# Kernel tuning notes

Hardware: AMD Instinct MI355X
Metric: run time of the kernel (lower is better)

Reference implementation:

```python
import jax, jax.numpy as jnp
import numpy as np

B, S, HID = 2, 2048, 4096
NH, NKV, HD = 32, 8, 128
GRP = NH // NKV          # query heads per kv head
G = 128                  # weight quant group size
FP8_MAX = 448.0          # e4m3 max
EPS = 1e-6


def _rmsnorm(x, w):
    return x * jax.lax.rsqrt(jnp.mean(x * x, axis=-1, keepdims=True) + EPS) * w


def _act_quant(x):
    # per-token fp8 quantization: scale = amax/448, values clipped to fp8 range
    s = jnp.max(jnp.abs(x), axis=-1, keepdims=True) / FP8_MAX
    s = jnp.maximum(s, 1e-6)
    return jnp.clip(x / s, -FP8_MAX, FP8_MAX), s


def _deq_weight(wi4, wscale):
    # wi4: [out, in] int values in [0,16) -> signed int4 [-8,7]
    # wscale: [out, in//G] per-group scales, broadcast along input dim
    return (wi4.astype(jnp.float32) - 8.0) * jnp.repeat(wscale, G, axis=1)


def _rotate_half(x):
    x1, x2 = jnp.split(x, 2, axis=-1)
    return jnp.concatenate([-x2, x1], axis=-1)


def setup_inputs() -> dict:
    key = jax.random.key(0)
    ks = jax.random.split(key, 8)
    hidden_states = jax.random.normal(ks[0], (B, S, HID), dtype=jnp.float32)
    ln_weight = jnp.ones((HID,), dtype=jnp.float32)
    # real RoPE tables
    inv_freq = 1.0 / (10000.0 ** (np.arange(0, HD, 2, dtype=np.float32) / HD))
    ang = np.arange(S, dtype=np.float32)[:, None] * inv_freq[None, :]
    emb = np.concatenate([ang, ang], axis=-1)  # [S, HD]
    cos = jnp.broadcast_to(jnp.asarray(np.cos(emb)), (B, S, HD)).astype(jnp.float32)
    sin = jnp.broadcast_to(jnp.asarray(np.sin(emb)), (B, S, HD)).astype(jnp.float32)
    def wq(k, out, inp):
        ki, ksc = jax.random.split(k)
        wi = jax.random.randint(ki, (out, inp), 0, 16, dtype=jnp.int32)
        sc = jax.random.uniform(ksc, (out, inp // G), dtype=jnp.float32) * 0.01 + 0.001
        return wi, sc
    wq_i4, wq_scale = wq(ks[1], NH * HD, HID)
    wk_i4, wk_scale = wq(ks[2], NKV * HD, HID)
    wv_i4, wv_scale = wq(ks[3], NKV * HD, HID)
    wo_i4, wo_scale = wq(ks[4], HID, NH * HD)
    return dict(hidden_states=hidden_states, ln_weight=ln_weight, cos=cos, sin=sin,
                wq_scale=wq_scale, wk_scale=wk_scale, wv_scale=wv_scale, wo_scale=wo_scale,
                wq_i4=wq_i4, wk_i4=wk_i4, wv_i4=wv_i4, wo_i4=wo_i4)


def reference(hidden_states, ln_weight, cos, sin,
              wq_scale, wk_scale, wv_scale, wo_scale,
              wq_i4, wk_i4, wv_i4, wo_i4):
    b, s, _ = hidden_states.shape
    residual = hidden_states
    h = _rmsnorm(hidden_states, ln_weight)
    qx, qx_s = _act_quant(h)                     # [b,s,HID], [b,s,1]
    q = (qx @ _deq_weight(wq_i4, wq_scale).T) * qx_s
    k = (qx @ _deq_weight(wk_i4, wk_scale).T) * qx_s
    v = (qx @ _deq_weight(wv_i4, wv_scale).T) * qx_s
    q = q.reshape(b, s, NH, HD)
    k = k.reshape(b, s, NKV, HD)
    v = v.reshape(b, s, NKV, HD)
    cse, sne = cos[:, :, None, :], sin[:, :, None, :]
    q = q * cse + _rotate_half(q) * sne
    k = k * cse + _rotate_half(k) * sne
    # GQA causal attention (fp8 fmha numerics emulated in fp32)
    qg = q.reshape(b, s, NKV, GRP, HD)
    scaling = HD ** -0.5
    scores = jnp.einsum('bskgd,btkd->bkgst', qg, k) * scaling  # [b,kv,g,s,t]
    causal = jnp.tril(jnp.ones((s, s), dtype=bool))
    scores = jnp.where(causal, scores, jnp.float32(-1e30))
    p = jax.nn.softmax(scores, axis=-1)
    o = jnp.einsum('bkgst,btkd->bskgd', p, v).reshape(b, s, NH * HD)
    qo, qo_s = _act_quant(o)
    out = (qo @ _deq_weight(wo_i4, wo_scale).T) * qo_s + residual
    return out
```

## Files before the change

kernel.cpp:

```cpp
#include <hip/hip_runtime.h>
#include <stdint.h>

#define HID    4096
#define SLEN   2048
#define BATCH  2
#define NHEADS 32
#define NKVH   8
#define HDIM   128
#define NTOK   (BATCH*SLEN)
#define NQK    (NHEADS*HDIM)
#define NKVD   (NKVH*HDIM)
#define NQKV   (NQK + 2*NKVD)
#define ASTR   (NQK + NKVD)

typedef unsigned short u16;
typedef short short8 __attribute__((ext_vector_type(8)));
typedef float f32x4 __attribute__((ext_vector_type(4)));
typedef int int4v __attribute__((ext_vector_type(4)));
typedef u16 u16x4 __attribute__((ext_vector_type(4)));

static __device__ __forceinline__ u16 f2bf(float f) {
  unsigned u = __builtin_bit_cast(unsigned, f);
  u += 0x7FFFu + ((u >> 16) & 1u);
  return (u16)(u >> 16);
}
static __device__ __forceinline__ float bf2f(u16 h) {
  return __builtin_bit_cast(float, (unsigned)h << 16);
}
static __device__ __forceinline__ void gload_lds16(const void* g, void* l) {
  __builtin_amdgcn_global_load_lds((const __attribute__((address_space(1))) void*)g,
                                   (__attribute__((address_space(3))) void*)l, 16, 0, 0);
}

__global__ __launch_bounds__(256) void k_rmsnorm(const float* __restrict__ x,
                                                 const float* __restrict__ w,
                                                 u16* __restrict__ h) {
  const int row = blockIdx.x;
  const float4* xr = (const float4*)(x + (size_t)row * HID);
  float4 vals[4];
  float ss = 0.f;
#pragma unroll
  for (int i = 0; i < 4; ++i) {
    float4 v = xr[threadIdx.x + i * 256];
    vals[i] = v;
    ss += v.x*v.x + v.y*v.y + v.z*v.z + v.w*v.w;
  }
#pragma unroll
  for (int off = 32; off; off >>= 1) ss += __shfl_xor(ss, off);
  __shared__ float red[4];
  if ((threadIdx.x & 63) == 0) red[threadIdx.x >> 6] = ss;
  __syncthreads();
  ss = red[0] + red[1] + red[2] + red[3];
  const float scale = rsqrtf(ss * (1.f / HID) + 1e-6f);
  u16* hr = h + (size_t)row * HID;
#pragma unroll
  for (int i = 0; i < 4; ++i) {
    int c = (threadIdx.x + i * 256) * 4;
    float4 v = vals[i];
    unsigned lo = (unsigned)f2bf(v.x * scale * w[c])   | ((unsigned)f2bf(v.y * scale * w[c+1]) << 16);
    unsigned hi = (unsigned)f2bf(v.z * scale * w[c+2]) | ((unsigned)f2bf(v.w * scale * w[c+3]) << 16);
    *(unsigned long long*)(hr + c) = ((unsigned long long)hi << 32) | lo;
  }
}

__global__ __launch_bounds__(256) void k_deq(const int* __restrict__ W,
                                             const float* __restrict__ Ws,
                                             u16* __restrict__ out) {
  const int idx = blockIdx.x * 256 + threadIdx.x;
  const int n = idx >> 9;
  const int k8 = (idx & 511) * 8;
  const float sc = Ws[n * 32 + (k8 >> 7)];
  int4v a = *(const int4v*)(W + (size_t)n * HID + k8);
  int4v b = *(const int4v*)(W + (size_t)n * HID + k8 + 4);
  u16 r[8];
#pragma unroll
  for (int j = 0; j < 4; ++j) r[j]     = f2bf((float)(a[j] - 8) * sc);
#pragma unroll
  for (int j = 0; j < 4; ++j) r[j + 4] = f2bf((float)(b[j] - 8) * sc);
  *(short8*)(out + (size_t)n * HID + k8) = *(short8*)r;
}

#define BM 128
#define BN 128
#define BK 64

__global__ __launch_bounds__(256) void k_gemm_qkv_b(
    const u16* __restrict__ A, const u16* __restrict__ B,
    u16* __restrict__ C, u16* __restrict__ Vt) {
  __shared__ __align__(16) u16 lA[BM * BK];
  __shared__ __align__(16) u16 lB[BN * BK];
  const int tid = threadIdx.x;
  const int lane = tid & 63;
  const int wave = tid >> 6;
  const int wm = wave >> 1, wn = wave & 1;
  const int m0 = blockIdx.x * BM;
  const int n0 = blockIdx.y * BN;

  const int rloc = wave * 8 + (lane >> 3);
  const int lb8 = (((lane & 7) ^ (lane >> 3)) << 3);

  f32x4 acc[4][4];
#pragma unroll
  for (int mi = 0; mi < 4; ++mi)
#pragma unroll
    for (int ni = 0; ni < 4; ++ni) acc[mi][ni] = (f32x4){0.f, 0.f, 0.f, 0.f};

  for (int k0 = 0; k0 < HID; k0 += BK) {
    __syncthreads();
#pragma unroll
    for (int p = 0; p < 4; ++p)
      gload_lds16(A + (size_t)(m0 + p * 32 + rloc) * HID + k0 + lb8,
                  lA + p * 2048 + wave * 512);
#pragma unroll
    for (int p = 0; p < 4; ++p)
      gload_lds16(B + (size_t)(n0 + p * 32 + rloc) * HID + k0 + lb8,
                  lB + p * 2048 + wave * 512);
    __syncthreads();
#pragma unroll
    for (int kc = 0; kc < 2; ++kc) {
      const int kOff = kc * 32 + ((lane >> 4) << 3);
      short8 af[4], bfr[4];
#pragma unroll
      for (int i = 0; i < 4; ++i) {
        const int m = wm * 64 + i * 16 + (lane & 15);
        af[i] = *(const short8*)(lA + ((m * 64 + kOff) ^ ((m & 7) << 3)));
        const int n = wn * 64 + i * 16 + (lane & 15);
        bfr[i] = *(const short8*)(lB + ((n * 64 + kOff) ^ ((n & 7) << 3)));
      }
#pragma unroll
      for (int mi = 0; mi < 4; ++mi)
#pragma unroll
        for (int ni = 0; ni < 4; ++ni)
          acc[mi][ni] = __builtin_amdgcn_mfma_f32_16x16x32_bf16(af[mi], bfr[ni], acc[mi][ni], 0, 0, 0);
    }
  }
  if (n0 < ASTR) {
#pragma unroll
    for (int mi = 0; mi < 4; ++mi) {
      const int row = m0 + wm * 64 + mi * 16 + ((lane >> 4) << 2);
#pragma unroll
      for (int ni = 0; ni < 4; ++ni) {
        const int col = n0 + wn * 64 + ni * 16 + (lane & 15);
#pragma unroll
        for (int r = 0; r < 4; ++r)
          C[(size_t)(row + r) * ASTR + col] = f2bf(acc[mi][ni][r]);
      }
    }
  } else {
#pragma unroll
    for (int mi = 0; mi < 4; ++mi) {
      const int row = m0 + wm * 64 + mi * 16 + ((lane >> 4) << 2);
      const int b_ = row >> 11, s_ = row & 2047;
#pragma unroll
      for (int ni = 0; ni < 4; ++ni) {
        const int colv = (n0 - ASTR) + wn * 64 + ni * 16 + (lane & 15);
        u16x4 pk;
#pragma unroll
        for (int r = 0; r < 4; ++r) pk[r] = f2bf(acc[mi][ni][r]);
        *(u16x4*)(Vt + ((size_t)(b_ * NKVH + (colv >> 7)) * HDIM + (colv & 127)) * SLEN + s_) = pk;
      }
    }
  }
}

__global__ __launch_bounds__(256) void k_gemm_o_b(
    const u16* __restrict__ A, const u16* __restrict__ B,
    const float* __restrict__ resid, float* __restrict__ out) {
  __shared__ __align__(16) u16 lA[BM * BK];
  __shared__ __align__(16) u16 lB[BN * BK];
  const int tid = threadIdx.x;
  const int lane = tid & 63;
  const int wave = tid >> 6;
  const int wm = wave >> 1, wn = wave & 1;
  const int m0 = blockIdx.x * BM;
  const int n0 = blockIdx.y * BN;

  const int rloc = wave * 8 + (lane >> 3);
  const int lb8 = (((lane & 7) ^ (lane >> 3)) << 3);

  f32x4 acc[4][4];
#pragma unroll
  for (int mi = 0; mi < 4; ++mi)
#pragma unroll
    for (int ni = 0; ni < 4; ++ni) acc[mi][ni] = (f32x4){0.f, 0.f, 0.f, 0.f};

  for (int k0 = 0; k0 < NQK; k0 += BK) {
    __syncthreads();
#pragma unroll
    for (int p = 0; p < 4; ++p)
      gload_lds16(A + (size_t)(m0 + p * 32 + rloc) * NQK + k0 + lb8,
                  lA + p * 2048 + wave * 512);
#pragma unroll
    for (int p = 0; p < 4; ++p)
      gload_lds16(B + (size_t)(n0 + p * 32 + rloc) * NQK + k0 + lb8,
                  lB + p * 2048 + wave * 512);
    __syncthreads();
#pragma unroll
    for (int kc = 0; kc < 2; ++kc) {
      const int kOff = kc * 32 + ((lane >> 4) << 3);
      short8 af[4], bfr[4];
#pragma unroll
      for (int i = 0; i < 4; ++i) {
        const int m = wm * 64 + i * 16 + (lane & 15);
        af[i] = *(const short8*)(lA + ((m * 64 + kOff) ^ ((m & 7) << 3)));
        const int n = wn * 64 + i * 16 + (lane & 15);
        bfr[i] = *(const short8*)(lB + ((n * 64 + kOff) ^ ((n & 7) << 3)));
      }
#pragma unroll
      for (int mi = 0; mi < 4; ++mi)
#pragma unroll
        for (int ni = 0; ni < 4; ++ni)
          acc[mi][ni] = __builtin_amdgcn_mfma_f32_16x16x32_bf16(af[mi], bfr[ni], acc[mi][ni], 0, 0, 0);
    }
  }
#pragma unroll
  for (int mi = 0; mi < 4; ++mi) {
    const int row = m0 + wm * 64 + mi * 16 + ((lane >> 4) << 2);
#pragma unroll
    for (int ni = 0; ni < 4; ++ni) {
      const int col = n0 + wn * 64 + ni * 16 + (lane & 15);
#pragma unroll
      for (int r = 0; r < 4; ++r) {
        const size_t idx = (size_t)(row + r) * HID + col;
        out[idx] = acc[mi][ni][r] + resid[idx];
      }
    }
  }
}

__global__ __launch_bounds__(256) void k_gemm_qkv(
    const u16* __restrict__ A,
    const int* __restrict__ Wq, const int* __restrict__ Wk, const int* __restrict__ Wv,
    const float* __restrict__ Sq, const float* __restrict__ Sk, const float* __restrict__ Sv,
    u16* __restrict__ C, u16* __restrict__ Vt) {
  __shared__ __align__(16) u16 lA[BM * BK];
  __shared__ __align__(16) u16 lB[BN * BK];
  const int tid = threadIdx.x;
  const int lane = tid & 63;
  const int wave = tid >> 6;
  const int wm = wave >> 1, wn = wave & 1;
  const int m0 = blockIdx.x * BM;
  const int n0 = blockIdx.y * BN;

  const int* W; const float* Ws; int nb;
  if (n0 < NQK)       { W = Wq; Ws = Sq; nb = n0; }
  else if (n0 < ASTR) { W = Wk; Ws = Sk; nb = n0 - NQK; }
  else                { W = Wv; Ws = Sv; nb = n0 - ASTR; }

  const int mloc = wave * 8 + (lane >> 3);
  const int lb8 = (((lane & 7) ^ (lane >> 3)) << 3);

  f32x4 acc[4][4];
#pragma unroll
  for (int mi = 0; mi < 4; ++mi)
#pragma unroll
    for (int ni = 0; ni < 4; ++ni) acc[mi][ni] = (f32x4){0.f, 0.f, 0.f, 0.f};

  for (int k0 = 0; k0 < HID; k0 += BK) {
    __syncthreads();
#pragma unroll
    for (int p = 0; p < 4; ++p)
      gload_lds16(A + (size_t)(m0 + p * 32 + mloc) * HID + k0 + lb8,
                  lA + p * 2048 + wave * 512);
    const int grp = k0 >> 7;
#pragma unroll
    for (int p = 0; p < 8; ++p) {
      const int n = p * 16 + (tid >> 4);
      const int kk = (tid & 15) * 4;
      int4v wv4 = *(const int4v*)(W + (size_t)(nb + n) * HID + k0 + kk);
      const float sc = Ws[(nb + n) * 32 + grp];
      unsigned lo = (unsigned)f2bf((float)(wv4[0] - 8) * sc) |
                    ((unsigned)f2bf((float)(wv4[1] - 8) * sc) << 16);
      unsigned hi = (unsigned)f2bf((float)(wv4[2] - 8) * sc) |
                    ((unsigned)f2bf((float)(wv4[3] - 8) * sc) << 16);
      const int di = (n * 64 + kk) ^ ((n & 7) << 3);
      unsigned* dst = (unsigned*)(lB + di);
      dst[0] = lo; dst[1] = hi;
    }
    __syncthreads();
#pragma unroll
    for (int kc = 0; kc < 2; ++kc) {
      const int kOff = kc * 32 + ((lane >> 4) << 3);
      short8 af[4], bfr[4];
#pragma unroll
      for (int i = 0; i < 4; ++i) {
        const int m = wm * 64 + i * 16 + (lane & 15);
        af[i] = *(const short8*)(lA + ((m * 64 + kOff) ^ ((m & 7) << 3)));
        const int n = wn * 64 + i * 16 + (lane & 15);
        bfr[i] = *(const short8*)(lB + ((n * 64 + kOff) ^ ((n & 7) << 3)));
      }
#pragma unroll
      for (int mi = 0; mi < 4; ++mi)
#pragma unroll
        for (int ni = 0; ni < 4; ++ni)
          acc[mi][ni] = __builtin_amdgcn_mfma_f32_16x16x32_bf16(af[mi], bfr[ni], acc[mi][ni], 0, 0, 0);
    }
  }
  if (n0 < ASTR) {
#pragma unroll
    for (int mi = 0; mi < 4; ++mi) {
      const int row = m0 + wm * 64 + mi * 16 + ((lane >> 4) << 2);
#pragma unroll
      for (int ni = 0; ni < 4; ++ni) {
        const int col = n0 + wn * 64 + ni * 16 + (lane & 15);
#pragma unroll
        for (int r = 0; r < 4; ++r)
          C[(size_t)(row + r) * ASTR + col] = f2bf(acc[mi][ni][r]);
      }
    }
  } else {
#pragma unroll
    for (int mi = 0; mi < 4; ++mi) {
      const int row = m0 + wm * 64 + mi * 16 + ((lane >> 4) << 2);
      const int b_ = row >> 11, s_ = row & 2047;
#pragma unroll
      for (int ni = 0; ni < 4; ++ni) {
        const int colv = (n0 - ASTR) + wn * 64 + ni * 16 + (lane & 15);
        u16x4 pk;
#pragma unroll
        for (int r = 0; r < 4; ++r) pk[r] = f2bf(acc[mi][ni][r]);
        *(u16x4*)(Vt + ((size_t)(b_ * NKVH + (colv >> 7)) * HDIM + (colv & 127)) * SLEN + s_) = pk;
      }
    }
  }
}

__global__ __launch_bounds__(256) void k_gemm_o(
    const u16* __restrict__ A, const int* __restrict__ W, const float* __restrict__ Ws,
    const float* __restrict__ resid, float* __restrict__ out) {
  __shared__ __align__(16) u16 lA[BM * BK];
  __shared__ __align__(16) u16 lB[BN * BK];
  const int tid = threadIdx.x;
  const int lane = tid & 63;
  const int wave = tid >> 6;
  const int wm = wave >> 1, wn = wave & 1;
  const int m0 = blockIdx.x * BM;
  const int n0 = blockIdx.y * BN;

  const int mloc = wave * 8 + (lane >> 3);
  const int lb8 = (((lane & 7) ^ (lane >> 3)) << 3);

  f32x4 acc[4][4];
#pragma unroll
  for (int mi = 0; mi < 4; ++mi)
#pragma unroll
    for (int ni = 0; ni < 4; ++ni) acc[mi][ni] = (f32x4){0.f, 0.f, 0.f, 0.f};

  for (int k0 = 0; k0 < NQK; k0 += BK) {
    __syncthreads();
#pragma unroll
    for (int p = 0; p < 4; ++p)
      gload_lds16(A + (size_t)(m0 + p * 32 + mloc) * NQK + k0 + lb8,
                  lA + p * 2048 + wave * 512);
    const int grp = k0 >> 7;
#pragma unroll
    for (int p = 0; p < 8; ++p) {
      const int n = p * 16 + (tid >> 4);
      const int kk = (tid & 15) * 4;
      int4v wv4 = *(const int4v*)(W + (size_t)(n0 + n) * NQK + k0 + kk);
      const float sc = Ws[(n0 + n) * 32 + grp];
      unsigned lo = (unsigned)f2bf((float)(wv4[0] - 8) * sc) |
                    ((unsigned)f2bf((float)(wv4[1] - 8) * sc) << 16);
      unsigned hi = (unsigned)f2bf((float)(wv4[2] - 8) * sc) |
                    ((unsigned)f2bf((float)(wv4[3] - 8) * sc) << 16);
      const int di = (n * 64 + kk) ^ ((n & 7) << 3);
      unsigned* dst = (unsigned*)(lB + di);
      dst[0] = lo; dst[1] = hi;
    }
    __syncthreads();
#pragma unroll
    for (int kc = 0; kc < 2; ++kc) {
      const int kOff = kc * 32 + ((lane >> 4) << 3);
      short8 af[4], bfr[4];
#pragma unroll
      for (int i = 0; i < 4; ++i) {
        const int m = wm * 64 + i * 16 + (lane & 15);
        af[i] = *(const short8*)(lA + ((m * 64 + kOff) ^ ((m & 7) << 3)));
        const int n = wn * 64 + i * 16 + (lane & 15);
        bfr[i] = *(const short8*)(lB + ((n * 64 + kOff) ^ ((n & 7) << 3)));
      }
#pragma unroll
      for (int mi = 0; mi < 4; ++mi)
#pragma unroll
        for (int ni = 0; ni < 4; ++ni)
          acc[mi][ni] = __builtin_amdgcn_mfma_f32_16x16x32_bf16(af[mi], bfr[ni], acc[mi][ni], 0, 0, 0);
      }
  }
#pragma unroll
  for (int mi = 0; mi < 4; ++mi) {
    const int row = m0 + wm * 64 + mi * 16 + ((lane >> 4) << 2);
#pragma unroll
    for (int ni = 0; ni < 4; ++ni) {
      const int col = n0 + wn * 64 + ni * 16 + (lane & 15);
#pragma unroll
      for (int r = 0; r < 4; ++r) {
        const size_t idx = (size_t)(row + r) * HID + col;
        out[idx] = acc[mi][ni][r] + resid[idx];
      }
    }
  }
}

__global__ __launch_bounds__(256) void k_rope(u16* __restrict__ qk,
                                              const float* __restrict__ cosb,
                                              const float* __restrict__ sinb) {
  const int idx = blockIdx.x * 256 + threadIdx.x;
  const int d = idx & 63;
  const int hh = (idx >> 6) % 40;
  const int t = idx / (64 * 40);
  const int col = (hh < 32) ? hh * HDIM : NQK + (hh - 32) * HDIM;
  u16* p = qk + (size_t)t * ASTR + col;
  const float c = cosb[t * HDIM + d], s = sinb[t * HDIM + d];
  const float x1 = bf2f(p[d]), x2 = bf2f(p[d + 64]);
  p[d]      = f2bf(x1 * c - x2 * s);
  p[d + 64] = f2bf(x2 * c + x1 * s);
}

__global__ __launch_bounds__(256) void k_attn(const u16* __restrict__ qk,
                                              const u16* __restrict__ vt,
                                              u16* __restrict__ o) {
  const int slot = blockIdx.x;
  const int w = (slot & 7) * 128 + (slot >> 3);
  const int qi = 15 - (w & 15);
  const int h = (w >> 4) & 31;
  const int b = w >> 9;
  const int kvh = h >> 2;
  const int q0 = qi * 128;
  const int lane = threadIdx.x & 63, wave = threadIdx.x >> 6;
  const int m = lane & 15, kg = lane >> 4;

  const u16* Qb = qk + (size_t)b * SLEN * ASTR + h * HDIM;
  const u16* Kb = qk + (size_t)b * SLEN * ASTR + NQK + kvh * HDIM;
  const u16* Vb = vt + (size_t)(b * NKVH + kvh) * HDIM * SLEN;

  __shared__ __align__(16) u16 Kt[64 * 128];
  __shared__ __align__(16) u16 Vts[128 * 64];
  __shared__ __align__(16) u16 Pl[4][32 * 72];

  const int qr = q0 + wave * 32;
  short8 qf[2][4];
#pragma unroll
  for (int mi = 0; mi < 2; ++mi)
#pragma unroll
    for (int kc = 0; kc < 4; ++kc)
      qf[mi][kc] = *(const short8*)(Qb + (size_t)(qr + mi * 16 + m) * ASTR + kc * 32 + kg * 8);

  f32x4 oacc[2][8];
#pragma unroll
  for (int mi = 0; mi < 2; ++mi)
#pragma unroll
    for (int n = 0; n < 8; ++n) oacc[mi][n] = (f32x4){0.f, 0.f, 0.f, 0.f};
  float rm[2][4], rl[2][4];
#pragma unroll
  for (int mi = 0; mi < 2; ++mi)
#pragma unroll
    for (int r = 0; r < 4; ++r) { rm[mi][r] = -3.0e38f; rl[mi][r] = 0.f; }

  const float sscale = 0.08838834764831845f;
  const int nt = q0 / 64 + 2;
  for (int t = 0; t < nt; ++t) {
    const int kv0 = t * 64;
    __syncthreads();
#pragma unroll
    for (int p = 0; p < 4; ++p) {
      const int row = p * 16 + wave * 4 + (lane >> 4);
      const int c8s = (lane & 15) ^ (row & 7);
      gload_lds16(Kb + (size_t)(kv0 + row) * ASTR + c8s * 8, Kt + p * 2048 + wave * 512);
    }
#pragma unroll
    for (int p = 0; p < 4; ++p) {
      const int d = p * 32 + wave * 8 + (lane >> 3);
      const int c8s = (lane & 7) ^ (d & 7);
      gload_lds16(Vb + (size_t)d * SLEN + kv0 + c8s * 8, Vts + p * 2048 + wave * 512);
    }
    __syncthreads();

    f32x4 sf[2][4];
#pragma unroll
    for (int mi = 0; mi < 2; ++mi)
#pragma unroll
      for (int ni = 0; ni < 4; ++ni) sf[mi][ni] = (f32x4){0.f, 0.f, 0.f, 0.f};
#pragma unroll
    for (int ni = 0; ni < 4; ++ni)
#pragma unroll
      for (int kc = 0; kc < 4; ++kc) {
        const int krow = ni * 16 + m;
        short8 kf = *(const short8*)(Kt + krow * 128 + (((kc * 4 + kg) ^ (krow & 7)) << 3));
#pragma unroll
        for (int mi = 0; mi < 2; ++mi)
          sf[mi][ni] = __builtin_amdgcn_mfma_f32_16x16x32_bf16(qf[mi][kc], kf, sf[mi][ni], 0, 0, 0);
      }

#pragma unroll
    for (int mi = 0; mi < 2; ++mi) {
      const bool dg = (kv0 + 63 > qr + mi * 16);
      float tmax[4] = {-3.0e38f, -3.0e38f, -3.0e38f, -3.0e38f};
#pragma unroll
      for (int ni = 0; ni < 4; ++ni)
#pragma unroll
        for (int r = 0; r < 4; ++r) {
          float s = sf[mi][ni][r] * sscale;
          if (dg) {
            const int rowg = qr + mi * 16 + kg * 4 + r;
            const int colg = kv0 + ni * 16 + m;
            if (colg > rowg) s = -1e30f;
          }
          sf[mi][ni][r] = s;
          tmax[r] = fmaxf(tmax[r], s);
        }
#pragma unroll
      for (int r = 0; r < 4; ++r)
#pragma unroll
        for (int off = 1; off < 16; off <<= 1)
          tmax[r] = fmaxf(tmax[r], __shfl_xor(tmax[r], off));
      float scl[4], psum[4];
#pragma unroll
      for (int r = 0; r < 4; ++r) {
        const float mn = fmaxf(rm[mi][r], tmax[r]);
        scl[r] = __expf(rm[mi][r] - mn);
        rm[mi][r] = mn;
        psum[r] = 0.f;
      }
#pragma unroll
      for (int ni = 0; ni < 4; ++ni)
#pragma unroll
        for (int r = 0; r < 4; ++r) {
          const float p = __expf(sf[mi][ni][r] - rm[mi][r]);
          psum[r] += p;
          Pl[wave][(mi * 16 + kg * 4 + r) * 72 + ni * 16 + m] = f2bf(p);
        }
#pragma unroll
      for (int r = 0; r < 4; ++r) {
#pragma unroll
        for (int off = 1; off < 16; off <<= 1)
          psum[r] += __shfl_xor(psum[r], off);
        rl[mi][r] = rl[mi][r] * scl[r] + psum[r];
      }
#pragma unroll
      for (int n = 0; n < 8; ++n)
#pragma unroll
        for (int r = 0; r < 4; ++r) oacc[mi][n][r] *= scl[r];
    }

#pragma unroll
    for (int kc = 0; kc < 2; ++kc) {
      short8 pf[2];
#pragma unroll
      for (int mi = 0; mi < 2; ++mi)
        pf[mi] = *(const short8*)(&Pl[wave][(mi * 16 + m) * 72 + kc * 32 + kg * 8]);
#pragma unroll
      for (int n = 0; n < 8; ++n) {
        const int vrow = n * 16 + m;
        short8 vf = *(const short8*)(Vts + vrow * 64 + (((kc * 4 + kg) ^ (vrow & 7)) << 3));
#pragma unroll
        for (int mi = 0; mi < 2; ++mi)
          oacc[mi][n] = __builtin_amdgcn_mfma_f32_16x16x32_bf16(pf[mi], vf, oacc[mi][n], 0, 0, 0);
      }
    }
  }

#pragma unroll
  for (int mi = 0; mi < 2; ++mi) {
    float inv[4];
#pragma unroll
    for (int r = 0; r < 4; ++r) inv[r] = 1.0f / rl[mi][r];
#pragma unroll
    for (int n = 0; n < 8; ++n)
#pragma unroll
      for (int r = 0; r < 4; ++r) {
        const int row = qr + mi * 16 + kg * 4 + r;
        o[((size_t)b * SLEN + row) * NQK + h * HDIM + n * 16 + m] = f2bf(oacc[mi][n][r] * inv[r]);
      }
  }
}

extern "C" void kernel_launch(void* const* d_in, const int* in_sizes, int n_in,
                              void* d_out, int out_size, void* d_ws, size_t ws_size,
                              hipStream_t stream) {
  (void)in_sizes; (void)n_in; (void)out_size;
  const float* x    = (const float*)d_in[0];
  const float* lnw  = (const float*)d_in[1];
  const float* cosb = (const float*)d_in[2];
  const float* sinb = (const float*)d_in[3];
  const float* sq   = (const float*)d_in[4];
  const float* sk   = (const float*)d_in[5];
  const float* sv   = (const float*)d_in[6];
  const float* so   = (const float*)d_in[7];
  const int* wq     = (const int*)d_in[8];
  const int* wk     = (const int*)d_in[9];
  const int* wv     = (const int*)d_in[10];
  const int* wo     = (const int*)d_in[11];

  u16* h   = (u16*)d_ws;
  u16* qkb = h + (size_t)NTOK * HID;
  u16* vtb = qkb + (size_t)NTOK * ASTR;
  u16* wqkvb = vtb + (size_t)BATCH * NKVH * HDIM * SLEN;
  u16* wob   = wqkvb + (size_t)NQKV * HID;
  float* out = (float*)d_out;

  const size_t need = ((size_t)NTOK * HID + (size_t)NTOK * ASTR +
                       (size_t)BATCH * NKVH * HDIM * SLEN +
                       (size_t)NQKV * HID + (size_t)HID * NQK) * sizeof(u16);
  const bool predeq = (ws_size >= need);

  k_rmsnorm<<<NTOK, 256, 0, stream>>>(x, lnw, h);

  if (predeq) {
    k_deq<<<NQK  * 2, 256, 0, stream>>>(wq, sq, wqkvb);
    k_deq<<<NKVD * 2, 256, 0, stream>>>(wk, sk, wqkvb + (size_t)NQK * HID);
    k_deq<<<NKVD * 2, 256, 0, stream>>>(wv, sv, wqkvb + (size_t)ASTR * HID);
    k_deq<<<NQK  * 2, 256, 0, stream>>>(wo, so, wob);
    dim3 g1(NTOK / BM, NQKV / BN);
    k_gemm_qkv_b<<<g1, 256, 0, stream>>>(h, wqkvb, qkb, vtb);
  } else {
    dim3 g1(NTOK / BM, NQKV / BN);
    k_gemm_qkv<<<g1, 256, 0, stream>>>(h, wq, wk, wv, sq, sk, sv, qkb, vtb);
  }

  k_rope<<<(NTOK * 40 * 64) / 256, 256, 0, stream>>>(qkb, cosb, sinb);

  k_attn<<<1024, 256, 0, stream>>>(qkb, vtb, h);

  dim3 g3(NTOK / BM, HID / BN);
  if (predeq) {
    k_gemm_o_b<<<g3, 256, 0, stream>>>(h, wob, x, out);
  } else {
    k_gemm_o<<<g3, 256, 0, stream>>>(h, wo, so, x, out);
  }
}
```

Baseline: 765.8 us.

## Double-buffer K/V tiles in attention, fold score scale into RoPE, merge deq launches

The attention kernel now prefetches the next K/V tile into a second LDS buffer while computing on the current one. It waits with vmcnt and raw barriers instead of two full syncthreads per tile. The P scratch buffer switches from padded rows to an XOR-swizzled layout. The softmax scale is folded into the RoPE pass for Q, so the per-element multiply in attention goes away. The four dequant launches are merged into one kernel. In exchange the kernel doubles K/V LDS use, which may lower occupancy, and Q is rounded to bf16 after scaling, which changes precision slightly.

```diff
diff --git a/kernel.cpp b/kernel.cpp
--- a/kernel.cpp
+++ b/kernel.cpp
@@ -63,21 +63,29 @@
   }
 }
 
-__global__ __launch_bounds__(256) void k_deq(const int* __restrict__ W,
-                                             const float* __restrict__ Ws,
-                                             u16* __restrict__ out) {
+__global__ __launch_bounds__(256) void k_deq_all(
+    const int* __restrict__ wq, const int* __restrict__ wk,
+    const int* __restrict__ wv, const int* __restrict__ wo,
+    const float* __restrict__ sq, const float* __restrict__ sk,
+    const float* __restrict__ sv, const float* __restrict__ so,
+    u16* __restrict__ out) {
   const int idx = blockIdx.x * 256 + threadIdx.x;
-  const int n = idx >> 9;
+  const int row = idx >> 9;
   const int k8 = (idx & 511) * 8;
-  const float sc = Ws[n * 32 + (k8 >> 7)];
-  int4v a = *(const int4v*)(W + (size_t)n * HID + k8);
-  int4v b = *(const int4v*)(W + (size_t)n * HID + k8 + 4);
-  u16 r[8];
-#pragma unroll
-  for (int j = 0; j < 4; ++j) r[j]     = f2bf((float)(a[j] - 8) * sc);
-#pragma unroll
-  for (int j = 0; j < 4; ++j) r[j + 4] = f2bf((float)(b[j] - 8) * sc);
-  *(short8*)(out + (size_t)n * HID + k8) = *(short8*)r;
+  const int* W; const float* S; int r;
+  if (row < 4096)      { W = wq; S = sq; r = row; }
+  else if (row < 5120) { W = wk; S = sk; r = row - 4096; }
+  else if (row < 6144) { W = wv; S = sv; r = row - 5120; }
+  else                 { W = wo; S = so; r = row - 6144; }
+  const float sc = S[r * 32 + (k8 >> 7)];
+  int4v a = *(const int4v*)(W + (size_t)r * HID + k8);
+  int4v b = *(const int4v*)(W + (size_t)r * HID + k8 + 4);
+  u16 rr[8];
+#pragma unroll
+  for (int j = 0; j < 4; ++j) rr[j]     = f2bf((float)(a[j] - 8) * sc);
+#pragma unroll
+  for (int j = 0; j < 4; ++j) rr[j + 4] = f2bf((float)(b[j] - 8) * sc);
+  *(short8*)(out + (size_t)row * HID + k8) = *(short8*)rr;
 }
 
 #define BM 128
@@ -409,12 +417,29 @@
   const int hh = (idx >> 6) % 40;
   const int t = idx / (64 * 40);
   const int col = (hh < 32) ? hh * HDIM : NQK + (hh - 32) * HDIM;
+  const float qs = (hh < 32) ? 0.08838834764831845f : 1.0f;
   u16* p = qk + (size_t)t * ASTR + col;
   const float c = cosb[t * HDIM + d], s = sinb[t * HDIM + d];
   const float x1 = bf2f(p[d]), x2 = bf2f(p[d + 64]);
-  p[d]      = f2bf(x1 * c - x2 * s);
-  p[d + 64] = f2bf(x2 * c + x1 * s);
-}
+  p[d]      = f2bf((x1 * c - x2 * s) * qs);
+  p[d + 64] = f2bf((x2 * c + x1 * s) * qs);
+}
+
+#define AVMW(n) asm volatile("s_waitcnt vmcnt(" #n ")" ::: "memory")
+#define ABAR()  __builtin_amdgcn_s_barrier(); asm volatile("" ::: "memory")
+
+#define STAGE_KV(buf, tt)                                                      \
+  { const int kv0_ = (tt) * 64;                                                \
+    _Pragma("unroll") for (int p = 0; p < 4; ++p) {                            \
+      const int row_ = p * 16 + wave * 4 + (lane >> 4);                        \
+      const int c8s_ = (lane & 15) ^ (row_ & 7);                               \
+      gload_lds16(Kb + (size_t)(kv0_ + row_) * ASTR + c8s_ * 8,                \
+                  Kt[buf] + p * 2048 + wave * 512); }                          \
+    _Pragma("unroll") for (int p = 0; p < 4; ++p) {                            \
+      const int d_ = p * 32 + wave * 8 + (lane >> 3);                          \
+      const int c8s_ = (lane & 7) ^ (d_ & 7);                                  \
+      gload_lds16(Vb + (size_t)d_ * SLEN + kv0_ + c8s_ * 8,                    \
+                  Vts[buf] + p * 2048 + wave * 512); } }
 
 __global__ __launch_bounds__(256) void k_attn(const u16* __restrict__ qk,
                                               const u16* __restrict__ vt,
@@ -433,9 +458,9 @@
   const u16* Kb = qk + (size_t)b * SLEN * ASTR + NQK + kvh * HDIM;
   const u16* Vb = vt + (size_t)(b * NKVH + kvh) * HDIM * SLEN;
 
-  __shared__ __align__(16) u16 Kt[64 * 128];
-  __shared__ __align__(16) u16 Vts[128 * 64];
-  __shared__ __align__(16) u16 Pl[4][32 * 72];
+  __shared__ __align__(16) u16 Kt[2][64 * 128];
+  __shared__ __align__(16) u16 Vts[2][128 * 64];
+  __shared__ __align__(16) u16 Pl[4][32 * 64];
 
   const int qr = q0 + wave * 32;
   short8 qf[2][4];
@@ -456,24 +481,18 @@
 #pragma unroll
     for (int r = 0; r < 4; ++r) { rm[mi][r] = -3.0e38f; rl[mi][r] = 0.f; }
 
-  const float sscale = 0.08838834764831845f;
   const int nt = q0 / 64 + 2;
+  STAGE_KV(0, 0);
   for (int t = 0; t < nt; ++t) {
     const int kv0 = t * 64;
-    __syncthreads();
-#pragma unroll
-    for (int p = 0; p < 4; ++p) {
-      const int row = p * 16 + wave * 4 + (lane >> 4);
-      const int c8s = (lane & 15) ^ (row & 7);
-      gload_lds16(Kb + (size_t)(kv0 + row) * ASTR + c8s * 8, Kt + p * 2048 + wave * 512);
-    }
-#pragma unroll
-    for (int p = 0; p < 4; ++p) {
-      const int d = p * 32 + wave * 8 + (lane >> 3);
-      const int c8s = (lane & 7) ^ (d & 7);
-      gload_lds16(Vb + (size_t)d * SLEN + kv0 + c8s * 8, Vts + p * 2048 + wave * 512);
-    }
-    __syncthreads();
+    const int cur = t & 1;
+    if (t + 1 < nt) {
+      STAGE_KV(cur ^ 1, t + 1);
+      AVMW(8);
+    } else {
+      AVMW(0);
+    }
+    ABAR();
 
     f32x4 sf[2][4];
 #pragma unroll
@@ -485,7 +504,7 @@
 #pragma unroll
       for (int kc = 0; kc < 4; ++kc) {
         const int krow = ni * 16 + m;
-        short8 kf = *(const short8*)(Kt + krow * 128 + (((kc * 4 + kg) ^ (krow & 7)) << 3));
+        short8 kf = *(const short8*)(Kt[cur] + krow * 128 + (((kc * 4 + kg) ^ (krow & 7)) << 3));
 #pragma unroll
         for (int mi = 0; mi < 2; ++mi)
           sf[mi][ni] = __builtin_amdgcn_mfma_f32_16x16x32_bf16(qf[mi][kc], kf, sf[mi][ni], 0, 0, 0);
@@ -499,7 +518,7 @@
       for (int ni = 0; ni < 4; ++ni)
 #pragma unroll
         for (int r = 0; r < 4; ++r) {
-          float s = sf[mi][ni][r] * sscale;
+          float s = sf[mi][ni][r];
           if (dg) {
             const int rowg = qr + mi * 16 + kg * 4 + r;
             const int colg = kv0 + ni * 16 + m;
@@ -527,7 +546,8 @@
         for (int r = 0; r < 4; ++r) {
           const float p = __expf(sf[mi][ni][r] - rm[mi][r]);
           psum[r] += p;
-          Pl[wave][(mi * 16 + kg * 4 + r) * 72 + ni * 16 + m] = f2bf(p);
+          const int prow = mi * 16 + kg * 4 + r;
+          Pl[wave][(prow << 6) + ((ni * 16 + m) ^ ((prow & 7) << 3))] = f2bf(p);
         }
 #pragma unroll
       for (int r = 0; r < 4; ++r) {
@@ -546,17 +566,20 @@
     for (int kc = 0; kc < 2; ++kc) {
       short8 pf[2];
 #pragma unroll
-      for (int mi = 0; mi < 2; ++mi)
-        pf[mi] = *(const short8*)(&Pl[wave][(mi * 16 + m) * 72 + kc * 32 + kg * 8]);
+      for (int mi = 0; mi < 2; ++mi) {
+        const int prow = mi * 16 + m;
+        pf[mi] = *(const short8*)(&Pl[wave][(prow << 6) + (((kc * 4 + kg) ^ (prow & 7)) << 3)]);
+      }
 #pragma unroll
       for (int n = 0; n < 8; ++n) {
         const int vrow = n * 16 + m;
-        short8 vf = *(const short8*)(Vts + vrow * 64 + (((kc * 4 + kg) ^ (vrow & 7)) << 3));
+        short8 vf = *(const short8*)(Vts[cur] + vrow * 64 + (((kc * 4 + kg) ^ (vrow & 7)) << 3));
 #pragma unroll
         for (int mi = 0; mi < 2; ++mi)
           oacc[mi][n] = __builtin_amdgcn_mfma_f32_16x16x32_bf16(pf[mi], vf, oacc[mi][n], 0, 0, 0);
       }
     }
+    ABAR();
   }
 
 #pragma unroll
@@ -606,10 +629,7 @@
   k_rmsnorm<<<NTOK, 256, 0, stream>>>(x, lnw, h);
 
   if (predeq) {
-    k_deq<<<NQK  * 2, 256, 0, stream>>>(wq, sq, wqkvb);
-    k_deq<<<NKVD * 2, 256, 0, stream>>>(wk, sk, wqkvb + (size_t)NQK * HID);
-    k_deq<<<NKVD * 2, 256, 0, stream>>>(wv, sv, wqkvb + (size_t)ASTR * HID);
-    k_deq<<<NQK  * 2, 256, 0, stream>>>(wo, so, wob);
+    k_deq_all<<<(10240 * 512) / 256, 256, 0, stream>>>(wq, wk, wv, wo, sq, sk, sv, so, wqkvb);
     dim3 g1(NTOK / BM, NQKV / BN);
     k_gemm_qkv_b<<<g1, 256, 0, stream>>>(h, wqkvb, qkb, vtb);
   } else {
@@ -621,10 +641,11 @@
 
   k_attn<<<1024, 256, 0, stream>>>(qkb, vtb, h);
 
-  dim3 g3(NTOK / BM, HID / BN);
   if (predeq) {
+    dim3 g3(NTOK / BM, HID / BN);
     k_gemm_o_b<<<g3, 256, 0, stream>>>(h, wob, x, out);
   } else {
+    dim3 g3(NTOK / BM, HID / BN);
     k_gemm_o<<<g3, 256, 0, stream>>>(h, wo, so, x, out);
   }
 }
```

Result: slower. 813.5 us (+6.2%).
